# Kernel optimization log

Hardware: AMD Instinct MI355X
Metric: run time of the kernel (lower is better)

Reference implementation:

```python
import jax, jax.numpy as jnp
import numpy as np

N = 30000        # num nodes
R = 16           # num relations
B = 30           # num bases (hard-coded in source)
E = 960000       # num edges (avg degree 32)
IN, HID, OUT, ADR = 128, 128, 64, 400


def setup_inputs() -> dict:
    key = jax.random.key(0)
    ks = jax.random.split(key, 13)
    s_in = 1.0 / np.sqrt(IN)
    s_hid = 1.0 / np.sqrt(HID)
    s_out = 1.0 / np.sqrt(OUT)
    return {
        "x": jax.random.normal(ks[0], (N, IN), jnp.float32),
        "edge_index": jax.random.randint(ks[1], (2, E), 0, N, jnp.int64),
        "edge_type": jax.random.randint(ks[2], (E,), 0, R, jnp.int64),
        "comp1": jax.random.normal(ks[3], (R, B), jnp.float32) * (1.0 / np.sqrt(B)),
        "basis1": jax.random.normal(ks[4], (B, IN, HID), jnp.float32) * s_in,
        "root1": jax.random.normal(ks[5], (IN, HID), jnp.float32) * s_in,
        "bias1": jnp.zeros((HID,), jnp.float32),
        "comp2": jax.random.normal(ks[6], (R, B), jnp.float32) * (1.0 / np.sqrt(B)),
        "basis2": jax.random.normal(ks[7], (B, HID, OUT), jnp.float32) * s_hid,
        "root2": jax.random.normal(ks[8], (HID, OUT), jnp.float32) * s_hid,
        "bias2": jnp.zeros((OUT,), jnp.float32),
        "wc": jax.random.normal(ks[9], (OUT, ADR), jnp.float32) * s_out,
        "bc": jnp.zeros((ADR,), jnp.float32),
    }


def _rgcn_conv(x, src, dst, etype, comp, basis, root, bias):
    """PyG RGCNConv: out[i] = sum_r mean_{e: dst=i, rel=r} x[src_e] @ W_r + x[i] @ root + bias,
    with basis decomposition W_r = sum_b comp[r,b] * basis[b].
    Aggregate-first: segment-mean x[src] into (node, relation) buckets, then contract."""
    n, din = x.shape
    seg = dst * R + etype                                   # [E] composite segment id
    msg = x[src]                                            # [E, din] edge gather
    sums = jax.ops.segment_sum(msg, seg, num_segments=n * R)            # [N*R, din]
    cnt = jax.ops.segment_sum(jnp.ones((src.shape[0],), x.dtype), seg,
                              num_segments=n * R)                       # [N*R]
    mean = sums / jnp.maximum(cnt, 1.0)[:, None]            # per-relation mean
    agg = mean.reshape(n, R, din)                           # [N, R, din]
    w = jnp.einsum('rb,bio->rio', comp, basis)              # [R, din, dout]
    return jnp.einsum('nri,rio->no', agg, w) + x @ root + bias


def reference(x, edge_index, edge_type, comp1, basis1, root1, bias1,
              comp2, basis2, root2, bias2, wc, bc):
    src, dst = edge_index[0], edge_index[1]
    h = _rgcn_conv(x, src, dst, edge_type, comp1, basis1, root1, bias1)
    h = jax.nn.relu(h)
    h = _rgcn_conv(h, src, dst, edge_type, comp2, basis2, root2, bias2)
    return h @ wc + bc
```

## Files before the change

kernel.cpp:

```cpp
#include <hip/hip_runtime.h>

#define R_    16
#define NBAS  30
#define DIN1  128
#define DHID  128
#define DOUT2 64
#define DADR  400
#define KCH   128
#define LDB   ((R_ + 1) * 128)

typedef __attribute__((ext_vector_type(8))) short bf16x8;
typedef __attribute__((ext_vector_type(4))) float f32x4;

__device__ __forceinline__ short f2bf(float f) {
    unsigned u = __float_as_uint(f);
    u += 0x7fffu + ((u >> 16) & 1u);
    return (short)(u >> 16);
}
__device__ __forceinline__ unsigned packbf(float lo, float hi) {
    return (unsigned)(unsigned short)f2bf(lo) | ((unsigned)(unsigned short)f2bf(hi) << 16);
}

struct Row8 { f32x4 lo, hi; };

__device__ __forceinline__ Row8 row8_zero() {
    Row8 z; z.lo = (f32x4){0.f,0.f,0.f,0.f}; z.hi = (f32x4){0.f,0.f,0.f,0.f}; return z;
}
__device__ __forceinline__ Row8 row8_add(Row8 a, int4 v) {
    unsigned u0 = (unsigned)v.x, u1 = (unsigned)v.y, u2 = (unsigned)v.z, u3 = (unsigned)v.w;
    a.lo[0] += __uint_as_float(u0 << 16);
    a.lo[1] += __uint_as_float(u0 & 0xffff0000u);
    a.lo[2] += __uint_as_float(u1 << 16);
    a.lo[3] += __uint_as_float(u1 & 0xffff0000u);
    a.hi[0] += __uint_as_float(u2 << 16);
    a.hi[1] += __uint_as_float(u2 & 0xffff0000u);
    a.hi[2] += __uint_as_float(u3 << 16);
    a.hi[3] += __uint_as_float(u3 & 0xffff0000u);
    return a;
}
__device__ __forceinline__ int4 row8_pack(Row8 a) {
    int4 o;
    o.x = (int)packbf(a.lo[0], a.lo[1]);
    o.y = (int)packbf(a.lo[2], a.lo[3]);
    o.z = (int)packbf(a.hi[0], a.hi[1]);
    o.w = (int)packbf(a.hi[2], a.hi[3]);
    return o;
}

__device__ __forceinline__ Row8 gather_row(const short* __restrict__ featbf,
                                           const int* __restrict__ off2,
                                           const int* __restrict__ srt,
                                           int r, int row, int N, int l16) {
    Row8 a = row8_zero();
    if (row >= N) return a;
    if (r < R_) {
        int seg = r * N + row;
        int b = off2[seg];
        int c = off2[seg + 1] - b;
        int s = c < 16 ? c : 16;
        int idx = (l16 < s) ? srt[b + l16] : 0;
        int j = 0;
        for (; j + 2 <= s; j += 2) {
            int i0 = __shfl(idx, j, 16);
            int i1 = __shfl(idx, j + 1, 16);
            int4 v0 = *(const int4*)(featbf + (size_t)i0 * KCH + l16 * 8);
            int4 v1 = *(const int4*)(featbf + (size_t)i1 * KCH + l16 * 8);
            a = row8_add(a, v0);
            a = row8_add(a, v1);
        }
        if (j < s) {
            int i0 = __shfl(idx, j, 16);
            a = row8_add(a, *(const int4*)(featbf + (size_t)i0 * KCH + l16 * 8));
        }
        for (int p = b + 16; p < b + c; ++p)
            a = row8_add(a, *(const int4*)(featbf + (size_t)srt[p] * KCH + l16 * 8));
        float sc = 1.f / (float)(c > 1 ? c : 1);
        a.lo *= sc; a.hi *= sc;
    } else {
        a = row8_add(a, *(const int4*)(featbf + (size_t)row * KCH + l16 * 8));
    }
    return a;
}

__global__ __launch_bounds__(256) void tobf_kernel(const float* __restrict__ in,
                                                   short* __restrict__ out, int n4) {
    int i = blockIdx.x * 256 + threadIdx.x;
    if (i >= n4) return;
    float4 v = ((const float4*)in)[i];
    short4 b = { f2bf(v.x), f2bf(v.y), f2bf(v.z), f2bf(v.w) };
    ((short4*)out)[i] = b;
}

__global__ __launch_bounds__(256) void count_kernel(const int* __restrict__ dst,
                                                    const int* __restrict__ ety,
                                                    int* __restrict__ cnt, int E, int N) {
    int e = blockIdx.x * blockDim.x + threadIdx.x;
    if (e < E) atomicAdd(&cnt[ety[e] * N + dst[e]], 1);
}

#define SCAN_CHUNK 2048
#define SCAN_IT    8

__global__ __launch_bounds__(256) void scan_bsum_kernel(const int* __restrict__ cnt, int nseg,
                                                        int* __restrict__ bsum) {
    __shared__ int sd[256];
    int base = blockIdx.x * SCAN_CHUNK;
    int s = 0;
    #pragma unroll
    for (int j = 0; j < SCAN_IT; ++j) {
        int idx = base + j * 256 + threadIdx.x;
        if (idx < nseg) s += cnt[idx];
    }
    sd[threadIdx.x] = s;
    __syncthreads();
    for (int st = 128; st > 0; st >>= 1) {
        if (threadIdx.x < st) sd[threadIdx.x] += sd[threadIdx.x + st];
        __syncthreads();
    }
    if (threadIdx.x == 0) bsum[blockIdx.x] = sd[0];
}

__global__ __launch_bounds__(256) void scan_top_kernel(const int* __restrict__ bsum, int nblk,
                                                       int* __restrict__ boff,
                                                       int* __restrict__ off, int nseg) {
    if (nblk > 256) {
        if (threadIdx.x == 0) {
            int run = 0;
            for (int i = 0; i < nblk; ++i) { int t = bsum[i]; boff[i] = run; run += t; }
            off[nseg] = run;
        }
        return;
    }
    __shared__ int sd[256];
    int v = (threadIdx.x < nblk) ? bsum[threadIdx.x] : 0;
    sd[threadIdx.x] = v;
    __syncthreads();
    for (int st = 1; st < 256; st <<= 1) {
        int t = (threadIdx.x >= st) ? sd[threadIdx.x - st] : 0;
        __syncthreads();
        sd[threadIdx.x] += t;
        __syncthreads();
    }
    if (threadIdx.x < nblk) boff[threadIdx.x] = sd[threadIdx.x] - v;
    if (threadIdx.x == nblk - 1) off[nseg] = sd[threadIdx.x];
}

__global__ __launch_bounds__(256) void scan_final_kernel(const int* __restrict__ cnt, int nseg,
                                                         const int* __restrict__ boff,
                                                         int* __restrict__ off,
                                                         int* __restrict__ cursor) {
    __shared__ int sd[256];
    int base = blockIdx.x * SCAN_CHUNK + threadIdx.x * SCAN_IT;
    int v[SCAN_IT];
    int s = 0;
    #pragma unroll
    for (int j = 0; j < SCAN_IT; ++j) {
        int idx = base + j;
        v[j] = (idx < nseg) ? cnt[idx] : 0;
        s += v[j];
    }
    sd[threadIdx.x] = s;
    __syncthreads();
    for (int st = 1; st < 256; st <<= 1) {
        int t = (threadIdx.x >= st) ? sd[threadIdx.x - st] : 0;
        __syncthreads();
        sd[threadIdx.x] += t;
        __syncthreads();
    }
    int run = boff[blockIdx.x] + sd[threadIdx.x] - s;
    #pragma unroll
    for (int j = 0; j < SCAN_IT; ++j) {
        int idx = base + j;
        if (idx < nseg) { off[idx] = run; cursor[idx] = run; }
        run += v[j];
    }
}

__global__ __launch_bounds__(256) void reorder_kernel(const int* __restrict__ src,
                                                      const int* __restrict__ dst,
                                                      const int* __restrict__ ety,
                                                      int* __restrict__ cursor,
                                                      int* __restrict__ srt, int E, int N) {
    int e = blockIdx.x * blockDim.x + threadIdx.x;
    if (e >= E) return;
    int seg = ety[e] * N + dst[e];
    int pos = atomicAdd(&cursor[seg], 1);
    srt[pos] = src[e];
}

#define PREP1 (R_ * DIN1 * DHID)
#define PREP2 (PREP1 + R_ * DHID * DOUT2)
#define PREP3 (PREP2 + DIN1 * DHID)
#define PREP4 (PREP3 + DHID * DOUT2)
#define PREP5 (PREP4 + DADR * DOUT2)
__global__ __launch_bounds__(256) void prep_kernel(const float* __restrict__ comp1,
                                                   const float* __restrict__ basis1,
                                                   const float* __restrict__ root1,
                                                   const float* __restrict__ comp2,
                                                   const float* __restrict__ basis2,
                                                   const float* __restrict__ root2,
                                                   const float* __restrict__ wc,
                                                   short* __restrict__ BT1,
                                                   short* __restrict__ BT2,
                                                   short* __restrict__ wcT) {
    int idx = blockIdx.x * 256 + threadIdx.x;
    if (idx < PREP1) {
        int o = idx % DHID, i = (idx / DHID) % DIN1, r = idx / (DHID * DIN1);
        float acc = 0.f;
        #pragma unroll 6
        for (int b = 0; b < NBAS; ++b)
            acc += comp1[r * NBAS + b] * basis1[((size_t)b * DIN1 + i) * DHID + o];
        BT1[(size_t)o * LDB + r * DIN1 + i] = f2bf(acc);
    } else if (idx < PREP2) {
        int t = idx - PREP1;
        int o = t % DOUT2, i = (t / DOUT2) % DHID, r = t / (DOUT2 * DHID);
        float acc = 0.f;
        #pragma unroll 6
        for (int b = 0; b < NBAS; ++b)
            acc += comp2[r * NBAS + b] * basis2[((size_t)b * DHID + i) * DOUT2 + o];
        BT2[(size_t)o * LDB + r * DHID + i] = f2bf(acc);
    } else if (idx < PREP3) {
        int t = idx - PREP2;
        int o = t % DHID, i = t / DHID;
        BT1[(size_t)o * LDB + R_ * DIN1 + i] = f2bf(root1[(size_t)i * DHID + o]);
    } else if (idx < PREP4) {
        int t = idx - PREP3;
        int o = t % DOUT2, i = t / DOUT2;
        BT2[(size_t)o * LDB + R_ * DHID + i] = f2bf(root2[(size_t)i * DOUT2 + o]);
    } else if (idx < PREP5) {
        int t = idx - PREP4;
        int a = t / DOUT2, k = t % DOUT2;
        wcT[(size_t)a * DOUT2 + k] = f2bf(wc[(size_t)k * DADR + a]);
    }
}

template<int BN, bool OUTBF>
__global__ __launch_bounds__(512, 6)
void rgcn_fused_kernel(const short* __restrict__ featbf,
                       const int* __restrict__ off2,
                       const int* __restrict__ srt,
                       const short* __restrict__ BT,
                       const float* __restrict__ bias,
                       void* __restrict__ Hout, int N, int relu)
{
    constexpr int BM = 32, BK = 128;
    constexpr int MR = (BN == 128) ? 2 : 1;
    constexpr int BL = BN / 32;

    __shared__ short lA[2][BM * BK];
    __shared__ short lB[BN * BK];

    const int tid  = threadIdx.x;
    const int lane = tid & 63;
    const int wv   = tid >> 6;
    const int g32  = tid >> 4;
    const int l16  = tid & 15;
    const int n0   = blockIdx.x * BM;
    const int row  = n0 + g32;

    const int colBase  = (BN == 128) ? wv * 16 : (wv & 3) * 16;
    const int rowTile0 = (BN == 128) ? 0 : (wv >> 2) * 16;

    f32x4 acc[MR];
    #pragma unroll
    for (int m = 0; m < MR; ++m)
        acc[m] = (f32x4){0.f, 0.f, 0.f, 0.f};

    const int abyte = ((g32 * BK + l16 * 8) << 1) ^ ((g32 & 15) << 4);

    {
        Row8 a = gather_row(featbf, off2, srt, 0, row, N, l16);
        *(int4*)((char*)lA[0] + abyte) = row8_pack(a);
    }

    for (int r = 0; r <= R_; ++r) {
        __syncthreads();

        #pragma unroll
        for (int j = 0; j < BL; ++j) {
            int o = j * 32 + g32;
            int4 v = *(const int4*)(BT + (size_t)o * LDB + r * BK + l16 * 8);
            int byte = ((o * BK + l16 * 8) << 1) ^ ((o & 15) << 4);
            *(int4*)((char*)lB + byte) = v;
        }

        Row8 an = row8_zero();
        if (r < R_) an = gather_row(featbf, off2, srt, r + 1, row, N, l16);

        __syncthreads();

        const char* lAc = (const char*)lA[r & 1];
        #pragma unroll
        for (int kk = 0; kk < BK / 32; ++kk) {
            const int kpos = kk * 32 + ((lane >> 4) << 3);
            const int bcol = colBase + (lane & 15);
            bf16x8 bfr = *(const bf16x8*)((const char*)lB +
                         (((bcol * BK + kpos) << 1) ^ ((bcol & 15) << 4)));
            #pragma unroll
            for (int m = 0; m < MR; ++m) {
                int arow = rowTile0 + m * 16 + (lane & 15);
                bf16x8 af = *(const bf16x8*)(lAc +
                             (((arow * BK + kpos) << 1) ^ ((arow & 15) << 4)));
                acc[m] = __builtin_amdgcn_mfma_f32_16x16x32_bf16(af, bfr, acc[m], 0, 0, 0);
            }
        }

        if (r < R_)
            *(int4*)((char*)lA[(r + 1) & 1] + abyte) = row8_pack(an);
    }

    #pragma unroll
    for (int m = 0; m < MR; ++m)
        #pragma unroll
        for (int i = 0; i < 4; ++i) {
            int rrow = rowTile0 + m * 16 + ((lane >> 4) << 2) + i;
            int col  = colBase + (lane & 15);
            int grow = n0 + rrow;
            if (grow >= N) continue;
            float v = acc[m][i] + bias[col];
            if (relu) v = fmaxf(v, 0.f);
            if (OUTBF) ((short*)Hout)[(size_t)grow * BN + col] = f2bf(v);
            else       ((float*)Hout)[(size_t)grow * BN + col] = v;
        }
}

__global__ __launch_bounds__(256)
void classifier_gemm_kernel(const short* __restrict__ h2bf,
                            const short* __restrict__ wcT,
                            const float* __restrict__ bc,
                            float* __restrict__ out, int N)
{
    constexpr int BM = 128, BN = 80, BK = 64;
    constexpr int MR = 2, NR = 5;

    __shared__ short lA[BM * BK];
    __shared__ short lB[BN * BK];

    const int tid  = threadIdx.x;
    const int lane = tid & 63;
    const int wv   = tid >> 6;
    const int nodeBase = blockIdx.x * BM;
    const int colBase  = blockIdx.y * BN;

    const int t8  = tid & 7;
    const int r32 = tid >> 3;

    #pragma unroll
    for (int it = 0; it < 4; ++it) {
        int row  = it * 32 + r32;
        int grow = nodeBase + row;
        int4 v = {0, 0, 0, 0};
        if (grow < N) v = *(const int4*)(h2bf + (size_t)grow * DOUT2 + t8 * 8);
        int byte = ((row * BK + t8 * 8) << 1) ^ ((row & 7) << 4);
        *(int4*)((char*)lA + byte) = v;
    }
    for (int o = r32; o < BN; o += 32) {
        int4 v = *(const int4*)(wcT + (size_t)(colBase + o) * DOUT2 + t8 * 8);
        int byte = ((o * BK + t8 * 8) << 1) ^ ((o & 7) << 4);
        *(int4*)((char*)lB + byte) = v;
    }
    __syncthreads();

    f32x4 acc[MR][NR];
    #pragma unroll
    for (int m = 0; m < MR; ++m)
        #pragma unroll
        for (int n = 0; n < NR; ++n)
            acc[m][n] = (f32x4){0.f, 0.f, 0.f, 0.f};

    #pragma unroll
    for (int kk = 0; kk < BK / 32; ++kk) {
        const int kpos = kk * 32 + (lane >> 4) * 8;
        bf16x8 af[MR], bfr[NR];
        #pragma unroll
        for (int m = 0; m < MR; ++m) {
            int row = wv * 32 + m * 16 + (lane & 15);
            af[m] = *(const bf16x8*)((const char*)lA +
                     (((row * BK + kpos) << 1) ^ ((row & 7) << 4)));
        }
        #pragma unroll
        for (int n = 0; n < NR; ++n) {
            int col = n * 16 + (lane & 15);
            bfr[n] = *(const bf16x8*)((const char*)lB +
                     (((col * BK + kpos) << 1) ^ ((col & 7) << 4)));
        }
        #pragma unroll
        for (int m = 0; m < MR; ++m)
            #pragma unroll
            for (int n = 0; n < NR; ++n)
                acc[m][n] = __builtin_amdgcn_mfma_f32_16x16x32_bf16(
                    af[m], bfr[n], acc[m][n], 0, 0, 0);
    }

    #pragma unroll
    for (int m = 0; m < MR; ++m)
        #pragma unroll
        for (int n = 0; n < NR; ++n)
            #pragma unroll
            for (int i = 0; i < 4; ++i) {
                int row  = wv * 32 + m * 16 + ((lane >> 4) << 2) + i;
                int col  = n * 16 + (lane & 15);
                int grow = nodeBase + row;
                if (grow >= N) continue;
                int gcol = colBase + col;
                out[(size_t)grow * DADR + gcol] = acc[m][n][i] + bc[gcol];
            }
}

static inline size_t align16(size_t x) { return (x + 15) & ~(size_t)15; }

extern "C" void kernel_launch(void* const* d_in, const int* in_sizes, int n_in,
                              void* d_out, int out_size, void* d_ws, size_t ws_size,
                              hipStream_t stream) {
    const float* x      = (const float*)d_in[0];
    const int*   ei     = (const int*)d_in[1];
    const int*   et     = (const int*)d_in[2];
    const float* comp1  = (const float*)d_in[3];
    const float* basis1 = (const float*)d_in[4];
    const float* root1  = (const float*)d_in[5];
    const float* bias1  = (const float*)d_in[6];
    const float* comp2  = (const float*)d_in[7];
    const float* basis2 = (const float*)d_in[8];
    const float* root2  = (const float*)d_in[9];
    const float* bias2  = (const float*)d_in[10];
    const float* wc     = (const float*)d_in[11];
    const float* bc     = (const float*)d_in[12];
    float* out = (float*)d_out;

    const int E = in_sizes[1] / 2;
    const int N = in_sizes[0] / DIN1;
    const int* srcp = ei;
    const int* dstp = ei + E;

    const int NSEG = N * R_;
    const int NBLK = (NSEG + SCAN_CHUNK - 1) / SCAN_CHUNK;

    char* ws = (char*)d_ws;
    size_t o = 0;
    int*   cntI   = (int*)(ws + o);   o = align16(o + (size_t)NSEG * 4);
    int*   off2   = (int*)(ws + o);   o = align16(o + (size_t)(NSEG + 1) * 4);
    int*   cursor = (int*)(ws + o);   o = align16(o + (size_t)NSEG * 4);
    int*   bsum   = (int*)(ws + o);   o = align16(o + (size_t)NBLK * 4);
    int*   boff   = (int*)(ws + o);   o = align16(o + (size_t)NBLK * 4);
    int*   srt    = (int*)(ws + o);   o = align16(o + (size_t)E * 4);
    short* BT1    = (short*)(ws + o); o = align16(o + (size_t)DHID * LDB * 2);
    short* BT2    = (short*)(ws + o); o = align16(o + (size_t)DOUT2 * LDB * 2);
    short* wcTb   = (short*)(ws + o); o = align16(o + (size_t)DADR * DOUT2 * 2);
    short* xbf    = (short*)(ws + o); o = align16(o + (size_t)N * DIN1 * 2);
    short* h1bf   = (short*)(ws + o); o = align16(o + (size_t)N * DHID * 2);
    short* h2bf   = (short*)(ws + o); o = align16(o + (size_t)N * DOUT2 * 2);

    const int n4 = N * DIN1 / 4;
    tobf_kernel<<<(n4 + 255) / 256, 256, 0, stream>>>(x, xbf, n4);

    hipMemsetAsync(cntI, 0, (size_t)NSEG * 4, stream);
    count_kernel<<<(E + 255) / 256, 256, 0, stream>>>(dstp, et, cntI, E, N);
    scan_bsum_kernel<<<NBLK, 256, 0, stream>>>(cntI, NSEG, bsum);
    scan_top_kernel<<<1, 256, 0, stream>>>(bsum, NBLK, boff, off2, NSEG);
    scan_final_kernel<<<NBLK, 256, 0, stream>>>(cntI, NSEG, boff, off2, cursor);
    reorder_kernel<<<(E + 255) / 256, 256, 0, stream>>>(srcp, dstp, et, cursor, srt, E, N);

    prep_kernel<<<(PREP5 + 255) / 256, 256, 0, stream>>>(comp1, basis1, root1,
                                                         comp2, basis2, root2, wc,
                                                         BT1, BT2, wcTb);

    const int gGrid = (N + 31) / 32;
    rgcn_fused_kernel<DHID, true><<<gGrid, 512, 0, stream>>>(xbf,  off2, srt, BT1, bias1, h1bf, N, 1);
    rgcn_fused_kernel<DOUT2, true><<<gGrid, 512, 0, stream>>>(h1bf, off2, srt, BT2, bias2, h2bf, N, 0);

    dim3 cGrid((N + 127) / 128, DADR / 80);
    classifier_gemm_kernel<<<cGrid, 256, 0, stream>>>(h2bf, wcTb, bc, out, N);
}
```

Measured before the change: 311.4 us.

## Pre-swizzle relation weights into MFMA fragment layout and load directly to registers

The prep kernel now writes the per-relation weight matrices in MFMA B-fragment order, so each wave loads its fragments straight from global memory into registers, prefetched one relation ahead. This removes the per-relation LDS staging of B and one of the two block barriers per relation iteration. The neighbor-gather loop is also unrolled by four to keep more row loads in flight, and the next relation's gather now runs after the current MFMAs instead of before them. Costs are more register pressure and B reloads from L2 by every wave instead of one shared LDS copy.

```diff
diff --git a/kernel.cpp b/kernel.cpp
--- a/kernel.cpp
+++ b/kernel.cpp
@@ -7,7 +7,6 @@
 #define DOUT2 64
 #define DADR  400
 #define KCH   128
-#define LDB   ((R_ + 1) * 128)
 
 typedef __attribute__((ext_vector_type(8))) short bf16x8;
 typedef __attribute__((ext_vector_type(4))) float f32x4;
@@ -47,10 +46,10 @@
     return o;
 }
 
-__device__ __forceinline__ Row8 gather_row(const short* __restrict__ featbf,
-                                           const int* __restrict__ off2,
-                                           const int* __restrict__ srt,
-                                           int r, int row, int N, int l16) {
+__device__ __forceinline__ Row8 gather_row4(const short* __restrict__ featbf,
+                                            const int* __restrict__ off2,
+                                            const int* __restrict__ srt,
+                                            int r, int row, int N, int l16) {
     Row8 a = row8_zero();
     if (row >= N) return a;
     if (r < R_) {
@@ -60,6 +59,20 @@
         int s = c < 16 ? c : 16;
         int idx = (l16 < s) ? srt[b + l16] : 0;
         int j = 0;
+        for (; j + 4 <= s; j += 4) {
+            int i0 = __shfl(idx, j, 16);
+            int i1 = __shfl(idx, j + 1, 16);
+            int i2 = __shfl(idx, j + 2, 16);
+            int i3 = __shfl(idx, j + 3, 16);
+            int4 v0 = *(const int4*)(featbf + (size_t)i0 * KCH + l16 * 8);
+            int4 v1 = *(const int4*)(featbf + (size_t)i1 * KCH + l16 * 8);
+            int4 v2 = *(const int4*)(featbf + (size_t)i2 * KCH + l16 * 8);
+            int4 v3 = *(const int4*)(featbf + (size_t)i3 * KCH + l16 * 8);
+            a = row8_add(a, v0);
+            a = row8_add(a, v1);
+            a = row8_add(a, v2);
+            a = row8_add(a, v3);
+        }
         for (; j + 2 <= s; j += 2) {
             int i0 = __shfl(idx, j, 16);
             int i1 = __shfl(idx, j + 1, 16);
@@ -186,6 +199,15 @@
     int seg = ety[e] * N + dst[e];
     int pos = atomicAdd(&cursor[seg], 1);
     srt[pos] = src[e];
+}
+
+__device__ __forceinline__ size_t fragidx(int r, int i, int o, int CT) {
+    int kk   = i >> 5;
+    int hi   = (i >> 3) & 3;
+    int j    = i & 7;
+    int lane = hi * 16 + (o & 15);
+    int ct   = o >> 4;
+    return ((((size_t)r * CT + ct) * 4 + kk) * 64 + lane) * 8 + j;
 }
 
 #define PREP1 (R_ * DIN1 * DHID)
@@ -200,8 +222,8 @@
                                                    const float* __restrict__ basis2,
                                                    const float* __restrict__ root2,
                                                    const float* __restrict__ wc,
-                                                   short* __restrict__ BT1,
-                                                   short* __restrict__ BT2,
+                                                   short* __restrict__ Bf1,
+                                                   short* __restrict__ Bf2,
                                                    short* __restrict__ wcT) {
     int idx = blockIdx.x * 256 + threadIdx.x;
     if (idx < PREP1) {
@@ -210,7 +232,7 @@
         #pragma unroll 6
         for (int b = 0; b < NBAS; ++b)
             acc += comp1[r * NBAS + b] * basis1[((size_t)b * DIN1 + i) * DHID + o];
-        BT1[(size_t)o * LDB + r * DIN1 + i] = f2bf(acc);
+        Bf1[fragidx(r, i, o, DHID / 16)] = f2bf(acc);
     } else if (idx < PREP2) {
         int t = idx - PREP1;
         int o = t % DOUT2, i = (t / DOUT2) % DHID, r = t / (DOUT2 * DHID);
@@ -218,15 +240,15 @@
         #pragma unroll 6
         for (int b = 0; b < NBAS; ++b)
             acc += comp2[r * NBAS + b] * basis2[((size_t)b * DHID + i) * DOUT2 + o];
-        BT2[(size_t)o * LDB + r * DHID + i] = f2bf(acc);
+        Bf2[fragidx(r, i, o, DOUT2 / 16)] = f2bf(acc);
     } else if (idx < PREP3) {
         int t = idx - PREP2;
         int o = t % DHID, i = t / DHID;
-        BT1[(size_t)o * LDB + R_ * DIN1 + i] = f2bf(root1[(size_t)i * DHID + o]);
+        Bf1[fragidx(R_, i, o, DHID / 16)] = f2bf(root1[(size_t)i * DHID + o]);
     } else if (idx < PREP4) {
         int t = idx - PREP3;
         int o = t % DOUT2, i = t / DOUT2;
-        BT2[(size_t)o * LDB + R_ * DHID + i] = f2bf(root2[(size_t)i * DOUT2 + o]);
+        Bf2[fragidx(R_, i, o, DOUT2 / 16)] = f2bf(root2[(size_t)i * DOUT2 + o]);
     } else if (idx < PREP5) {
         int t = idx - PREP4;
         int a = t / DOUT2, k = t % DOUT2;
@@ -239,16 +261,16 @@
 void rgcn_fused_kernel(const short* __restrict__ featbf,
                        const int* __restrict__ off2,
                        const int* __restrict__ srt,
-                       const short* __restrict__ BT,
+                       const short* __restrict__ Bf,
                        const float* __restrict__ bias,
                        void* __restrict__ Hout, int N, int relu)
 {
     constexpr int BM = 32, BK = 128;
+    constexpr int CT = BN / 16;
     constexpr int MR = (BN == 128) ? 2 : 1;
-    constexpr int BL = BN / 32;
+    constexpr int CHSTRIDE = CT * 2048;
 
     __shared__ short lA[2][BM * BK];
-    __shared__ short lB[BN * BK];
 
     const int tid  = threadIdx.x;
     const int lane = tid & 63;
@@ -258,7 +280,7 @@
     const int n0   = blockIdx.x * BM;
     const int row  = n0 + g32;
 
-    const int colBase  = (BN == 128) ? wv * 16 : (wv & 3) * 16;
+    const int ct       = (BN == 128) ? wv : (wv & 3);
     const int rowTile0 = (BN == 128) ? 0 : (wv >> 2) * 16;
 
     f32x4 acc[MR];
@@ -267,46 +289,50 @@
         acc[m] = (f32x4){0.f, 0.f, 0.f, 0.f};
 
     const int abyte = ((g32 * BK + l16 * 8) << 1) ^ ((g32 & 15) << 4);
+    const short* Bfw = Bf + (size_t)ct * 2048 + (size_t)lane * 8;
 
     {
-        Row8 a = gather_row(featbf, off2, srt, 0, row, N, l16);
+        Row8 a = gather_row4(featbf, off2, srt, 0, row, N, l16);
         *(int4*)((char*)lA[0] + abyte) = row8_pack(a);
     }
+    bf16x8 bfr0 = *(const bf16x8*)(Bfw + 0 * 512);
+    bf16x8 bfr1 = *(const bf16x8*)(Bfw + 1 * 512);
+    bf16x8 bfr2 = *(const bf16x8*)(Bfw + 2 * 512);
+    bf16x8 bfr3 = *(const bf16x8*)(Bfw + 3 * 512);
+    __syncthreads();
 
     for (int r = 0; r <= R_; ++r) {
-        __syncthreads();
-
-        #pragma unroll
-        for (int j = 0; j < BL; ++j) {
-            int o = j * 32 + g32;
-            int4 v = *(const int4*)(BT + (size_t)o * LDB + r * BK + l16 * 8);
-            int byte = ((o * BK + l16 * 8) << 1) ^ ((o & 15) << 4);
-            *(int4*)((char*)lB + byte) = v;
-        }
-
-        Row8 an = row8_zero();
-        if (r < R_) an = gather_row(featbf, off2, srt, r + 1, row, N, l16);
-
-        __syncthreads();
-
-        const char* lAc = (const char*)lA[r & 1];
-        #pragma unroll
-        for (int kk = 0; kk < BK / 32; ++kk) {
-            const int kpos = kk * 32 + ((lane >> 4) << 3);
-            const int bcol = colBase + (lane & 15);
-            bf16x8 bfr = *(const bf16x8*)((const char*)lB +
-                         (((bcol * BK + kpos) << 1) ^ ((bcol & 15) << 4)));
+        bf16x8 nf0, nf1, nf2, nf3;
+        if (r < R_) {
+            const short* p = Bfw + (size_t)(r + 1) * CHSTRIDE;
+            nf0 = *(const bf16x8*)(p + 0 * 512);
+            nf1 = *(const bf16x8*)(p + 1 * 512);
+            nf2 = *(const bf16x8*)(p + 2 * 512);
+            nf3 = *(const bf16x8*)(p + 3 * 512);
+        }
+
+        {
+            const char* lAc = (const char*)lA[r & 1];
             #pragma unroll
-            for (int m = 0; m < MR; ++m) {
-                int arow = rowTile0 + m * 16 + (lane & 15);
-                bf16x8 af = *(const bf16x8*)(lAc +
-                             (((arow * BK + kpos) << 1) ^ ((arow & 15) << 4)));
-                acc[m] = __builtin_amdgcn_mfma_f32_16x16x32_bf16(af, bfr, acc[m], 0, 0, 0);
+            for (int kk = 0; kk < 4; ++kk) {
+                const int kpos = kk * 32 + ((lane >> 4) << 3);
+                bf16x8 bfr = (kk == 0) ? bfr0 : (kk == 1) ? bfr1 : (kk == 2) ? bfr2 : bfr3;
+                #pragma unroll
+                for (int m = 0; m < MR; ++m) {
+                    int arow = rowTile0 + m * 16 + (lane & 15);
+                    bf16x8 af = *(const bf16x8*)(lAc +
+                                 (((arow * BK + kpos) << 1) ^ ((arow & 15) << 4)));
+                    acc[m] = __builtin_amdgcn_mfma_f32_16x16x32_bf16(af, bfr, acc[m], 0, 0, 0);
+                }
             }
         }
 
-        if (r < R_)
+        if (r < R_) {
+            Row8 an = gather_row4(featbf, off2, srt, r + 1, row, N, l16);
             *(int4*)((char*)lA[(r + 1) & 1] + abyte) = row8_pack(an);
+        }
+        __syncthreads();
+        bfr0 = nf0; bfr1 = nf1; bfr2 = nf2; bfr3 = nf3;
     }
 
     #pragma unroll
@@ -314,7 +340,7 @@
         #pragma unroll
         for (int i = 0; i < 4; ++i) {
             int rrow = rowTile0 + m * 16 + ((lane >> 4) << 2) + i;
-            int col  = colBase + (lane & 15);
+            int col  = ct * 16 + (lane & 15);
             int grow = n0 + rrow;
             if (grow >= N) continue;
             float v = acc[m][i] + bias[col];
@@ -443,8 +469,8 @@
     int*   bsum   = (int*)(ws + o);   o = align16(o + (size_t)NBLK * 4);
     int*   boff   = (int*)(ws + o);   o = align16(o + (size_t)NBLK * 4);
     int*   srt    = (int*)(ws + o);   o = align16(o + (size_t)E * 4);
-    short* BT1    = (short*)(ws + o); o = align16(o + (size_t)DHID * LDB * 2);
-    short* BT2    = (short*)(ws + o); o = align16(o + (size_t)DOUT2 * LDB * 2);
+    short* Bf1    = (short*)(ws + o); o = align16(o + (size_t)(R_ + 1) * DIN1 * DHID * 2);
+    short* Bf2    = (short*)(ws + o); o = align16(o + (size_t)(R_ + 1) * DHID * DOUT2 * 2);
     short* wcTb   = (short*)(ws + o); o = align16(o + (size_t)DADR * DOUT2 * 2);
     short* xbf    = (short*)(ws + o); o = align16(o + (size_t)N * DIN1 * 2);
     short* h1bf   = (short*)(ws + o); o = align16(o + (size_t)N * DHID * 2);
@@ -462,11 +488,11 @@
 
     prep_kernel<<<(PREP5 + 255) / 256, 256, 0, stream>>>(comp1, basis1, root1,
                                                          comp2, basis2, root2, wc,
-                                                         BT1, BT2, wcTb);
+                                                         Bf1, Bf2, wcTb);
 
     const int gGrid = (N + 31) / 32;
-    rgcn_fused_kernel<DHID, true><<<gGrid, 512, 0, stream>>>(xbf,  off2, srt, BT1, bias1, h1bf, N, 1);
-    rgcn_fused_kernel<DOUT2, true><<<gGrid, 512, 0, stream>>>(h1bf, off2, srt, BT2, bias2, h2bf, N, 0);
+    rgcn_fused_kernel<DHID, true><<<gGrid, 512, 0, stream>>>(xbf,  off2, srt, Bf1, bias1, h1bf, N, 1);
+    rgcn_fused_kernel<DOUT2, true><<<gGrid, 512, 0, stream>>>(h1bf, off2, srt, Bf2, bias2, h2bf, N, 0);
 
     dim3 cGrid((N + 127) / 128, DADR / 80);
     classifier_gemm_kernel<<<cGrid, 256, 0, stream>>>(h2bf, wcTb, bc, out, N);
```

Result: slower. 342.5 us (+10.0%).
